# Optimization experiments

Hardware: AMD Instinct MI355X
Metric: run time of the kernel (lower is better)

## Reference

```python
import jax, jax.numpy as jnp
import numpy as np

EPS = 1e-7

def _masked_stats(x, w, k):
    # Parallel equivalent of the sequential Welford update_counter loop:
    # after the loop, mean = running mean, s = sum of squared deviations (M2),
    # std = sqrt(s / (k - 1)). Computed under no_grad in torch -> stop_gradient.
    m = jnp.sum(x * w, axis=0) / k
    s = jnp.sum(w * (x - m) ** 2, axis=0)
    std = jnp.sqrt(s / (k - 1.0))
    return jax.lax.stop_gradient(m), jax.lax.stop_gradient(std)

def _mlp(x, W1, b1, W2, b2):
    # MlpClass(d, d, 2*d, n_hidden=1) with relu act: d -> 2d -> d
    return jax.nn.relu(x @ W1 + b1) @ W2 + b2

def setup_inputs() -> dict:
    key = jax.random.key(0)
    ks = jax.random.split(key, 8)
    B, S, XD, DD = 8, 2048, 1024, 4096
    scale = 0.02
    return {
        "u": jax.random.normal(ks[0], (B, S, XD), jnp.float32),
        "v": jax.random.normal(ks[1], (B, S, DD), jnp.float32),
        "u_W1": jax.random.normal(ks[2], (XD, 2 * XD), jnp.float32) * scale,
        "u_b1": jnp.zeros((2 * XD,), jnp.float32),
        "u_W2": jax.random.normal(ks[3], (2 * XD, XD), jnp.float32) * scale,
        "u_b2": jnp.zeros((XD,), jnp.float32),
        "v_W1": jax.random.normal(ks[4], (DD, 2 * DD), jnp.float32) * scale,
        "v_b1": jnp.zeros((2 * DD,), jnp.float32),
        "v_W2": jax.random.normal(ks[5], (2 * DD, DD), jnp.float32) * scale,
        "v_b2": jnp.zeros((DD,), jnp.float32),
    }

def reference(u, v, u_W1, u_b1, u_W2, u_b2, v_W1, v_b1, v_W2, v_b2):
    u_ = u.reshape(-1, u.shape[-1]).astype(jnp.float32)  # [N, x_dim]
    v_ = v.reshape(-1, v.shape[-1]).astype(jnp.float32)  # [N, delta_dim]
    # nonzero-row mask; torch drops masked rows, we zero them (equivalent math,
    # static shapes). With randn inputs no row is masked.
    nz = jnp.any(u_ != 0, axis=-1) & jnp.any(v_ != 0, axis=-1)
    w = nz.astype(u_.dtype)[:, None]  # [N, 1]
    k = jnp.sum(w)
    u_mean, u_std = _masked_stats(u_, w, k)
    v_mean, v_std = _masked_stats(v_, w, k)
    u_input = (u_ - u_mean) / (u_std + EPS)
    v_input = (v_ - v_mean) / (v_std + EPS)
    out1 = _mlp(u_input, u_W1, u_b1, u_W2, u_b2) * w
    out2 = _mlp(v_input, v_W1, v_b1, v_W2, v_b2) * w
    return out1, out2
```

## Files before the change

### kernel.cpp

```cpp
#include <hip/hip_runtime.h>
#include <hip/hip_bf16.h>

#define NROWS 16384
#define XD 1024
#define DD 4096

typedef __attribute__((ext_vector_type(8))) short short8;
typedef __attribute__((ext_vector_type(4))) float f32x4;

__device__ __forceinline__ unsigned short f2bf(float f) {
  unsigned int u = __builtin_bit_cast(unsigned int, f);
  u += 0x7fffu + ((u >> 16) & 1u);
  return (unsigned short)(u >> 16);
}

__device__ __forceinline__ void load_lds16(const void* g, void* l) {
  __builtin_amdgcn_global_load_lds((const __attribute__((address_space(1))) void*)g,
                                   (__attribute__((address_space(3))) void*)l, 16, 0, 0);
}

__global__ __launch_bounds__(256) void mask_kernel(const float* __restrict__ u,
                                                   const float* __restrict__ v,
                                                   float* __restrict__ w) {
  int r = blockIdx.x;
  int t = threadIdx.x;
  const f32x4* up = (const f32x4*)(u + (size_t)r * XD);
  const f32x4* vp = (const f32x4*)(v + (size_t)r * DD);
  f32x4 a = up[t];
  int fu = __syncthreads_or((a.x != 0.f) | (a.y != 0.f) | (a.z != 0.f) | (a.w != 0.f));
  int fv = 0;
#pragma unroll
  for (int it = 0; it < DD / (256 * 4); ++it) {
    if (!fv) {
      f32x4 b = vp[it * 256 + t];
      fv = __syncthreads_or((b.x != 0.f) | (b.y != 0.f) | (b.z != 0.f) | (b.w != 0.f));
    }
  }
  if (t == 0) w[r] = (fu && fv) ? 1.f : 0.f;
}

__global__ __launch_bounds__(256) void ksum_kernel(const float* __restrict__ w,
                                                   float* __restrict__ kout) {
  __shared__ float sm[256];
  float s = 0.f;
  for (int i = threadIdx.x; i < NROWS; i += 256) s += w[i];
  sm[threadIdx.x] = s;
  __syncthreads();
  for (int st = 128; st > 0; st >>= 1) {
    if (threadIdx.x < st) sm[threadIdx.x] += sm[threadIdx.x + st];
    __syncthreads();
  }
  if (threadIdx.x == 0) kout[0] = sm[0];
}

__global__ __launch_bounds__(256) void colstats_partial(const float* __restrict__ X, int cols,
                                                        const float* __restrict__ w,
                                                        float* __restrict__ p1,
                                                        float* __restrict__ p2) {
  int c = blockIdx.x * 256 + threadIdx.x;
  int r0 = blockIdx.y * (NROWS / 64);
  float s1 = 0.f, s2 = 0.f;
  for (int r = r0; r < r0 + NROWS / 64; ++r) {
    float wr = w[r];
    float x = X[(size_t)r * cols + c];
    float xw = x * wr;
    s1 += xw;
    s2 += xw * x;
  }
  p1[(size_t)blockIdx.y * cols + c] = s1;
  p2[(size_t)blockIdx.y * cols + c] = s2;
}

__global__ __launch_bounds__(256) void colstats_final(const float* __restrict__ p1,
                                                      const float* __restrict__ p2,
                                                      const float* __restrict__ kptr, int cols,
                                                      float* __restrict__ mean,
                                                      float* __restrict__ inv) {
  int c = blockIdx.x * 256 + threadIdx.x;
  float s1 = 0.f, s2 = 0.f;
  for (int j = 0; j < 64; ++j) {
    s1 += p1[(size_t)j * cols + c];
    s2 += p2[(size_t)j * cols + c];
  }
  float k = kptr[0];
  float m = s1 / k;
  float s = s2 - s1 * s1 / k;
  float sd = sqrtf(fmaxf(s, 0.f) / (k - 1.f));
  mean[c] = m;
  inv[c] = 1.f / (sd + 1e-7f);
}

__global__ __launch_bounds__(256) void wt_kernel(const float* __restrict__ W, int R, int C,
                                                 unsigned short* __restrict__ T) {
  __shared__ unsigned short tile[64][65];
  int r0 = blockIdx.x * 64, c0 = blockIdx.y * 64;
  int tr = threadIdx.x >> 2;
  int tc = (threadIdx.x & 3) * 16;
  const float* src = W + (size_t)(r0 + tr) * C + c0 + tc;
#pragma unroll
  for (int i = 0; i < 16; i += 4) {
    f32x4 v4 = *(const f32x4*)(src + i);
    tile[tr][tc + i + 0] = f2bf(v4.x);
    tile[tr][tc + i + 1] = f2bf(v4.y);
    tile[tr][tc + i + 2] = f2bf(v4.z);
    tile[tr][tc + i + 3] = f2bf(v4.w);
  }
  __syncthreads();
  unsigned short* dst = T + (size_t)(c0 + tr) * R + r0 + tc;
  short8 o0, o1;
#pragma unroll
  for (int i = 0; i < 8; ++i) o0[i] = (short)tile[tc + i][tr];
#pragma unroll
  for (int i = 0; i < 8; ++i) o1[i] = (short)tile[tc + 8 + i][tr];
  *(short8*)(dst) = o0;
  *(short8*)(dst + 8) = o1;
}

__global__ __launch_bounds__(256) void norm_kernel(const float* __restrict__ X,
                                                   const float* __restrict__ mean,
                                                   const float* __restrict__ inv,
                                                   unsigned short* __restrict__ O,
                                                   int colmask, size_t n8) {
  size_t stride = (size_t)gridDim.x * 256;
  for (size_t i = (size_t)blockIdx.x * 256 + threadIdx.x; i < n8; i += stride) {
    int c8 = (int)(i & (size_t)colmask);
    const float* xp = X + i * 8;
    f32x4 a = *(const f32x4*)xp;
    f32x4 b = *(const f32x4*)(xp + 4);
    f32x4 m0 = *(const f32x4*)(mean + c8 * 8);
    f32x4 m1 = *(const f32x4*)(mean + c8 * 8 + 4);
    f32x4 i0 = *(const f32x4*)(inv + c8 * 8);
    f32x4 i1 = *(const f32x4*)(inv + c8 * 8 + 4);
    short8 p;
    p[0] = (short)f2bf((a.x - m0.x) * i0.x);
    p[1] = (short)f2bf((a.y - m0.y) * i0.y);
    p[2] = (short)f2bf((a.z - m0.z) * i0.z);
    p[3] = (short)f2bf((a.w - m0.w) * i0.w);
    p[4] = (short)f2bf((b.x - m1.x) * i1.x);
    p[5] = (short)f2bf((b.y - m1.y) * i1.y);
    p[6] = (short)f2bf((b.z - m1.z) * i1.z);
    p[7] = (short)f2bf((b.w - m1.w) * i1.w);
    *(short8*)(O + i * 8) = p;
  }
}

template <int EPI>
__global__ __launch_bounds__(1024, 4) void gemm8p(const unsigned short* __restrict__ A,
                                                  const unsigned short* __restrict__ Bt,
                                                  const float* __restrict__ bias,
                                                  const float* __restrict__ wrow,
                                                  void* __restrict__ OutP,
                                                  int N, int K) {
  __shared__ char lds[131072];
  const int tid = threadIdx.x;
  const int lane = tid & 63;
  const int wave = tid >> 6;
  const int wm = wave >> 2;
  const int wn = wave & 3;

  const int gn = N >> 8;
  const int nwg = gridDim.x;
  const int gm = nwg / gn;
  const int bid = blockIdx.x;
  const int sw = (nwg & 7) ? bid : ((bid & 7) * (nwg >> 3) + (bid >> 3));
  const int SW_W = (gn >= 8) ? 8 : gn;
  const int SW_H = 32 / SW_W;
  int mt, nt;
  if ((gn % SW_W) == 0 && (gm % SW_H) == 0) {
    const int stn = gn / SW_W;
    const int st = sw >> 5;
    const int wi = sw & 31;
    mt = (st / stn) * SW_H + wi / SW_W;
    nt = (st % stn) * SW_W + wi % SW_W;
  } else {
    mt = sw / gn;
    nt = sw % gn;
  }
  const int m0 = mt << 8;
  const int n0 = nt << 8;

  const int srow = tid >> 3;
  const int scol = (((tid & 7) ^ (srow & 7)) << 3);

  const int NT = K >> 6;
  f32x4 acc[4][4] = {};

  const int fr = lane & 15;
  const int kbyte = (lane >> 4) << 4;

#define STAGE(T, BUF)                                                                   \
  {                                                                                     \
    const int k0_ = (T) << 6;                                                           \
    _Pragma("unroll") for (int i = 0; i < 2; ++i) {                                     \
      const int row_ = srow + i * 128;                                                  \
      load_lds16(A + (size_t)(m0 + row_) * K + k0_ + scol,                              \
                 lds + (BUF)*65536 + i * 16384 + tid * 16);                             \
      load_lds16(Bt + (size_t)(n0 + row_) * K + k0_ + scol,                             \
                 lds + (BUF)*65536 + 32768 + i * 16384 + tid * 16);                     \
    }                                                                                   \
  }

  STAGE(0, 0);
  __syncthreads();

  short8 af[4], bf_[4];
  for (int t = 0; t < NT; ++t) {
    const int buf = t & 1;
    const char* Ab = lds + buf * 65536;
    const char* Bb = lds + buf * 65536 + 32768;
    if (t + 1 < NT) STAGE(t + 1, buf ^ 1);

#pragma unroll
    for (int s = 0; s < 2; ++s) {
#pragma unroll
      for (int f = 0; f < 4; ++f) {
        const int r = wm * 64 + f * 16 + fr;
        af[f] = *(const short8*)(Ab + r * 128 + ((s * 64 + kbyte) ^ ((r & 7) << 4)));
      }
#pragma unroll
      for (int g = 0; g < 4; ++g) {
        const int r = wn * 64 + g * 16 + fr;
        bf_[g] = *(const short8*)(Bb + r * 128 + ((s * 64 + kbyte) ^ ((r & 7) << 4)));
      }
      __builtin_amdgcn_s_setprio(1);
#pragma unroll
      for (int f = 0; f < 4; ++f)
#pragma unroll
        for (int g = 0; g < 4; ++g)
          acc[f][g] = __builtin_amdgcn_mfma_f32_16x16x32_bf16(af[f], bf_[g], acc[f][g], 0, 0, 0);
      __builtin_amdgcn_s_setprio(0);
    }
    __syncthreads();
  }
#undef STAGE

  const int colloc = wn * 64 + fr;
  const int rowb = wm * 64 + ((lane >> 4) << 2);
  if (EPI == 0) {
    unsigned short* H = (unsigned short*)OutP;
#pragma unroll
    for (int f = 0; f < 4; ++f)
#pragma unroll
      for (int g = 0; g < 4; ++g) {
        const int c = n0 + colloc + g * 16;
        const float b = bias[c];
#pragma unroll
        for (int r = 0; r < 4; ++r) {
          const int row = m0 + rowb + f * 16 + r;
          H[(size_t)row * N + c] = f2bf(fmaxf(acc[f][g][r] + b, 0.f));
        }
      }
  } else {
    float* O = (float*)OutP;
#pragma unroll
    for (int f = 0; f < 4; ++f)
#pragma unroll
      for (int g = 0; g < 4; ++g) {
        const int c = n0 + colloc + g * 16;
        const float b = bias[c];
#pragma unroll
        for (int r = 0; r < 4; ++r) {
          const int row = m0 + rowb + f * 16 + r;
          O[(size_t)row * N + c] = (acc[f][g][r] + b) * wrow[row];
        }
      }
  }
}

extern "C" void kernel_launch(void* const* d_in, const int* in_sizes, int n_in,
                              void* d_out, int out_size, void* d_ws, size_t ws_size,
                              hipStream_t stream) {
  const float* u    = (const float*)d_in[0];
  const float* v    = (const float*)d_in[1];
  const float* u_W1 = (const float*)d_in[2];
  const float* u_b1 = (const float*)d_in[3];
  const float* u_W2 = (const float*)d_in[4];
  const float* u_b2 = (const float*)d_in[5];
  const float* v_W1 = (const float*)d_in[6];
  const float* v_b1 = (const float*)d_in[7];
  const float* v_W2 = (const float*)d_in[8];
  const float* v_b2 = (const float*)d_in[9];
  float* out1 = (float*)d_out;
  float* out2 = out1 + (size_t)NROWS * XD;

  float* wsf = (float*)d_ws;
  size_t off = 0;
  float* w_     = wsf + off; off += NROWS;
  float* kv     = wsf + off; off += 16;
  float* u_mean = wsf + off; off += XD;
  float* u_inv  = wsf + off; off += XD;
  float* v_mean = wsf + off; off += DD;
  float* v_inv  = wsf + off; off += DD;
  float* p1u    = wsf + off; off += 64 * XD;
  float* p2u    = wsf + off; off += 64 * XD;
  float* p1v    = wsf + off; off += 64 * DD;
  float* p2v    = wsf + off; off += 64 * DD;

  size_t boff = (off * 4 + 255) & ~(size_t)255;
  unsigned short* W1Tu = (unsigned short*)((char*)d_ws + boff); boff += (size_t)(2 * XD) * XD * 2;
  unsigned short* W2Tu = (unsigned short*)((char*)d_ws + boff); boff += (size_t)XD * (2 * XD) * 2;
  unsigned short* W1Tv = (unsigned short*)((char*)d_ws + boff); boff += (size_t)(2 * DD) * DD * 2;
  unsigned short* W2Tv = (unsigned short*)((char*)d_ws + boff); boff += (size_t)DD * (2 * DD) * 2;
  size_t fixedB = (boff + 255) & ~(size_t)255;

  static const int chs[7] = {16384, 8192, 4096, 2048, 1024, 512, 256};
  int CHu = 256, CHv = 256;
  double best = 1e30;
  for (int a = 0; a < 7; ++a)
    for (int b = 0; b < 7; ++b) {
      int cu = chs[a], cv = chs[b];
      size_t need = fixedB + (size_t)cu * XD * 6 + (size_t)cv * DD * 6 + 1024;
      if (need > ws_size) continue;
      auto util = [](int nwg) { return nwg >= 256 ? 1.0 : nwg / 256.0; };
      double cost = 68.75 / util((cu >> 8) * 8) + 68.75 / util((cu >> 8) * 4) +
                    550.0 / util((cv >> 8) * 32) + 550.0 / util((cv >> 8) * 16);
      if (cost < best) { best = cost; CHu = cu; CHv = cv; }
    }

  size_t p = fixedB;
  unsigned short* unc  = (unsigned short*)((char*)d_ws + p); p += (size_t)CHu * XD * 2;
  unsigned short* uhid = (unsigned short*)((char*)d_ws + p); p += (size_t)CHu * (2 * XD) * 2;
  unsigned short* vnc  = (unsigned short*)((char*)d_ws + p); p += (size_t)CHv * DD * 2;
  unsigned short* vhid = (unsigned short*)((char*)d_ws + p);

  mask_kernel<<<NROWS, 256, 0, stream>>>(u, v, w_);
  ksum_kernel<<<1, 256, 0, stream>>>(w_, kv);
  colstats_partial<<<dim3(XD / 256, 64), 256, 0, stream>>>(u, XD, w_, p1u, p2u);
  colstats_partial<<<dim3(DD / 256, 64), 256, 0, stream>>>(v, DD, w_, p1v, p2v);
  colstats_final<<<XD / 256, 256, 0, stream>>>(p1u, p2u, kv, XD, u_mean, u_inv);
  colstats_final<<<DD / 256, 256, 0, stream>>>(p1v, p2v, kv, DD, v_mean, v_inv);

  wt_kernel<<<dim3(XD / 64, (2 * XD) / 64), 256, 0, stream>>>(u_W1, XD, 2 * XD, W1Tu);
  wt_kernel<<<dim3((2 * XD) / 64, XD / 64), 256, 0, stream>>>(u_W2, 2 * XD, XD, W2Tu);
  wt_kernel<<<dim3(DD / 64, (2 * DD) / 64), 256, 0, stream>>>(v_W1, DD, 2 * DD, W1Tv);
  wt_kernel<<<dim3((2 * DD) / 64, DD / 64), 256, 0, stream>>>(v_W2, 2 * DD, DD, W2Tv);

  for (int r0 = 0; r0 < NROWS; r0 += CHu) {
    size_t n8 = (size_t)CHu * XD / 8;
    int ng = (int)(n8 / 256 < 2048 ? n8 / 256 : 2048);
    norm_kernel<<<ng, 256, 0, stream>>>(u + (size_t)r0 * XD, u_mean, u_inv, unc, XD / 8 - 1, n8);
    gemm8p<0><<<(CHu >> 8) * ((2 * XD) >> 8), 1024, 0, stream>>>(unc, W1Tu, u_b1, nullptr, uhid,
                                                                 2 * XD, XD);
    gemm8p<1><<<(CHu >> 8) * (XD >> 8), 1024, 0, stream>>>(uhid, W2Tu, u_b2, w_ + r0,
                                                           out1 + (size_t)r0 * XD, XD, 2 * XD);
  }
  for (int r0 = 0; r0 < NROWS; r0 += CHv) {
    size_t n8 = (size_t)CHv * DD / 8;
    int ng = (int)(n8 / 256 < 2048 ? n8 / 256 : 2048);
    norm_kernel<<<ng, 256, 0, stream>>>(v + (size_t)r0 * DD, v_mean, v_inv, vnc, DD / 8 - 1, n8);
    gemm8p<0><<<(CHv >> 8) * ((2 * DD) >> 8), 1024, 0, stream>>>(vnc, W1Tv, v_b1, nullptr, vhid,
                                                                 2 * DD, DD);
    gemm8p<1><<<(CHv >> 8) * (DD >> 8), 1024, 0, stream>>>(vhid, W2Tv, v_b2, w_ + r0,
                                                           out2 + (size_t)r0 * DD, DD, 2 * DD);
  }
}
```

Measured before the change: 2.271 ms.

## Load B fragments directly from global memory and remap workgroup tile swizzle

The GEMM kernel stops staging the B (weight) tile through LDS. Each wave now reads its B fragments straight from global memory into registers, which halves LDS use to 64KB per block. The tile-to-workgroup mapping also changes: when possible it uses tall 32-row M strips per N column, so a B tile stays hot in cache across consecutive workgroups. This trades LDS traffic and capacity for global and L2 load latency that the double-buffered loop does not hide for B.

```diff
diff --git a/kernel.cpp b/kernel.cpp
--- a/kernel.cpp
+++ b/kernel.cpp
@@ -145,13 +145,13 @@
 }
 
 template <int EPI>
-__global__ __launch_bounds__(1024, 4) void gemm8p(const unsigned short* __restrict__ A,
+__global__ __launch_bounds__(1024, 4) void gemmbg(const unsigned short* __restrict__ A,
                                                   const unsigned short* __restrict__ Bt,
                                                   const float* __restrict__ bias,
                                                   const float* __restrict__ wrow,
                                                   void* __restrict__ OutP,
                                                   int N, int K) {
-  __shared__ char lds[131072];
+  __shared__ char lds[65536];
   const int tid = threadIdx.x;
   const int lane = tid & 63;
   const int wave = tid >> 6;
@@ -163,15 +163,18 @@
   const int gm = nwg / gn;
   const int bid = blockIdx.x;
   const int sw = (nwg & 7) ? bid : ((bid & 7) * (nwg >> 3) + (bid >> 3));
-  const int SW_W = (gn >= 8) ? 8 : gn;
-  const int SW_H = 32 / SW_W;
   int mt, nt;
-  if ((gn % SW_W) == 0 && (gm % SW_H) == 0) {
-    const int stn = gn / SW_W;
+  if ((nwg & 7) == 0 && (gm & 31) == 0) {
     const int st = sw >> 5;
     const int wi = sw & 31;
-    mt = (st / stn) * SW_H + wi / SW_W;
-    nt = (st % stn) * SW_W + wi % SW_W;
+    mt = (st / gn) * 32 + wi;
+    nt = st % gn;
+  } else if ((nwg & 7) == 0 && (gn & 7) == 0 && (gm & 3) == 0) {
+    const int stn = gn >> 3;
+    const int st = sw >> 5;
+    const int wi = sw & 31;
+    mt = (st / stn) * 4 + (wi >> 3);
+    nt = (st % stn) * 8 + (wi & 7);
   } else {
     mt = sw / gn;
     nt = sw % gn;
@@ -187,6 +190,7 @@
 
   const int fr = lane & 15;
   const int kbyte = (lane >> 4) << 4;
+  const unsigned short* bbase = Bt + (size_t)(n0 + wn * 64 + fr) * K + ((lane >> 4) << 3);
 
 #define STAGE(T, BUF)                                                                   \
   {                                                                                     \
@@ -194,9 +198,7 @@
     _Pragma("unroll") for (int i = 0; i < 2; ++i) {                                     \
       const int row_ = srow + i * 128;                                                  \
       load_lds16(A + (size_t)(m0 + row_) * K + k0_ + scol,                              \
-                 lds + (BUF)*65536 + i * 16384 + tid * 16);                             \
-      load_lds16(Bt + (size_t)(n0 + row_) * K + k0_ + scol,                             \
-                 lds + (BUF)*65536 + 32768 + i * 16384 + tid * 16);                     \
+                 lds + (BUF)*32768 + i * 16384 + tid * 16);                             \
     }                                                                                   \
   }
 
@@ -206,21 +208,18 @@
   short8 af[4], bf_[4];
   for (int t = 0; t < NT; ++t) {
     const int buf = t & 1;
-    const char* Ab = lds + buf * 65536;
-    const char* Bb = lds + buf * 65536 + 32768;
+    const char* Ab = lds + buf * 32768;
     if (t + 1 < NT) STAGE(t + 1, buf ^ 1);
 
 #pragma unroll
     for (int s = 0; s < 2; ++s) {
+#pragma unroll
+      for (int g = 0; g < 4; ++g)
+        bf_[g] = *(const short8*)(bbase + (size_t)(g * 16) * K + ((t << 6) + s * 32));
 #pragma unroll
       for (int f = 0; f < 4; ++f) {
         const int r = wm * 64 + f * 16 + fr;
         af[f] = *(const short8*)(Ab + r * 128 + ((s * 64 + kbyte) ^ ((r & 7) << 4)));
-      }
-#pragma unroll
-      for (int g = 0; g < 4; ++g) {
-        const int r = wn * 64 + g * 16 + fr;
-        bf_[g] = *(const short8*)(Bb + r * 128 + ((s * 64 + kbyte) ^ ((r & 7) << 4)));
       }
       __builtin_amdgcn_s_setprio(1);
 #pragma unroll
@@ -339,18 +338,18 @@
     size_t n8 = (size_t)CHu * XD / 8;
     int ng = (int)(n8 / 256 < 2048 ? n8 / 256 : 2048);
     norm_kernel<<<ng, 256, 0, stream>>>(u + (size_t)r0 * XD, u_mean, u_inv, unc, XD / 8 - 1, n8);
-    gemm8p<0><<<(CHu >> 8) * ((2 * XD) >> 8), 1024, 0, stream>>>(unc, W1Tu, u_b1, nullptr, uhid,
+    gemmbg<0><<<(CHu >> 8) * ((2 * XD) >> 8), 1024, 0, stream>>>(unc, W1Tu, u_b1, nullptr, uhid,
                                                                  2 * XD, XD);
-    gemm8p<1><<<(CHu >> 8) * (XD >> 8), 1024, 0, stream>>>(uhid, W2Tu, u_b2, w_ + r0,
+    gemmbg<1><<<(CHu >> 8) * (XD >> 8), 1024, 0, stream>>>(uhid, W2Tu, u_b2, w_ + r0,
                                                            out1 + (size_t)r0 * XD, XD, 2 * XD);
   }
   for (int r0 = 0; r0 < NROWS; r0 += CHv) {
     size_t n8 = (size_t)CHv * DD / 8;
     int ng = (int)(n8 / 256 < 2048 ? n8 / 256 : 2048);
     norm_kernel<<<ng, 256, 0, stream>>>(v + (size_t)r0 * DD, v_mean, v_inv, vnc, DD / 8 - 1, n8);
-    gemm8p<0><<<(CHv >> 8) * ((2 * DD) >> 8), 1024, 0, stream>>>(vnc, W1Tv, v_b1, nullptr, vhid,
+    gemmbg<0><<<(CHv >> 8) * ((2 * DD) >> 8), 1024, 0, stream>>>(vnc, W1Tv, v_b1, nullptr, vhid,
                                                                  2 * DD, DD);
-    gemm8p<1><<<(CHv >> 8) * (DD >> 8), 1024, 0, stream>>>(vhid, W2Tv, v_b2, w_ + r0,
+    gemmbg<1><<<(CHv >> 8) * (DD >> 8), 1024, 0, stream>>>(vhid, W2Tv, v_b2, w_ + r0,
                                                            out2 + (size_t)r0 * DD, DD, 2 * DD);
   }
 }
```

Measured after the change: 5.525 ms. 143% more time.

## Replace 256x256 GEMM tile with 256x128 tile, K-step 32, 512 threads

Applied to the files above, without the earlier changes.

The bf16 MFMA GEMM moves from 1024-thread 256x256 tiles with a 64-wide K step and 128KB LDS to 512-thread 256x128 tiles with a 32-wide K step and 48KB LDS. It also adds a new LDS swizzle and row interleave for the smaller K slice. The goal is more workgroups per GPU and more resident blocks per CU for better occupancy and latency hiding. The chunk-size cost model is updated for the doubled grid. The trade-off is lower arithmetic intensity per tile, more global traffic for A, and twice as many K iterations, each followed by a barrier.

```diff
diff --git a/kernel.cpp b/kernel.cpp
--- a/kernel.cpp
+++ b/kernel.cpp
@@ -145,20 +145,20 @@
 }
 
 template <int EPI>
-__global__ __launch_bounds__(1024, 4) void gemm8p(const unsigned short* __restrict__ A,
-                                                  const unsigned short* __restrict__ Bt,
-                                                  const float* __restrict__ bias,
-                                                  const float* __restrict__ wrow,
-                                                  void* __restrict__ OutP,
-                                                  int N, int K) {
-  __shared__ char lds[131072];
+__global__ __launch_bounds__(512, 4) void gemm2b(const unsigned short* __restrict__ A,
+                                                 const unsigned short* __restrict__ Bt,
+                                                 const float* __restrict__ bias,
+                                                 const float* __restrict__ wrow,
+                                                 void* __restrict__ OutP,
+                                                 int N, int K) {
+  __shared__ char lds[49152];
   const int tid = threadIdx.x;
   const int lane = tid & 63;
   const int wave = tid >> 6;
-  const int wm = wave >> 2;
-  const int wn = wave & 3;
-
-  const int gn = N >> 8;
+  const int wm = wave >> 1;
+  const int wn = wave & 1;
+
+  const int gn = N >> 7;
   const int nwg = gridDim.x;
   const int gm = nwg / gn;
   const int bid = blockIdx.x;
@@ -177,27 +177,27 @@
     nt = sw % gn;
   }
   const int m0 = mt << 8;
-  const int n0 = nt << 8;
-
-  const int srow = tid >> 3;
-  const int scol = (((tid & 7) ^ (srow & 7)) << 3);
-
-  const int NT = K >> 6;
+  const int n0 = nt << 7;
+
+  const int srow = 2 * (tid >> 3) + ((tid >> 2) & 1);
+  const int sksl = (((tid & 3) ^ ((tid >> 3) & 3)) << 3);
+
+  const int NT = K >> 5;
   f32x4 acc[4][4] = {};
 
   const int fr = lane & 15;
-  const int kbyte = (lane >> 4) << 4;
-
-#define STAGE(T, BUF)                                                                   \
-  {                                                                                     \
-    const int k0_ = (T) << 6;                                                           \
-    _Pragma("unroll") for (int i = 0; i < 2; ++i) {                                     \
-      const int row_ = srow + i * 128;                                                  \
-      load_lds16(A + (size_t)(m0 + row_) * K + k0_ + scol,                              \
-                 lds + (BUF)*65536 + i * 16384 + tid * 16);                             \
-      load_lds16(Bt + (size_t)(n0 + row_) * K + k0_ + scol,                             \
-                 lds + (BUF)*65536 + 32768 + i * 16384 + tid * 16);                     \
-    }                                                                                   \
+  const int kg = lane >> 4;
+  const int fo = (fr >> 1) * 128 + (fr & 1) * 64 + (((kg ^ ((fr >> 1) & 3))) << 4);
+
+#define STAGE(T, BUF)                                                              \
+  {                                                                                \
+    const int k0_ = (T) << 5;                                                      \
+    load_lds16(A + (size_t)(m0 + srow) * K + k0_ + sksl,                           \
+               lds + (BUF)*16384 + tid * 16);                                      \
+    load_lds16(A + (size_t)(m0 + srow + 128) * K + k0_ + sksl,                     \
+               lds + (BUF)*16384 + 8192 + tid * 16);                               \
+    load_lds16(Bt + (size_t)(n0 + srow) * K + k0_ + sksl,                          \
+               lds + 32768 + (BUF)*8192 + tid * 16);                               \
   }
 
   STAGE(0, 0);
@@ -206,36 +206,27 @@
   short8 af[4], bf_[4];
   for (int t = 0; t < NT; ++t) {
     const int buf = t & 1;
-    const char* Ab = lds + buf * 65536;
-    const char* Bb = lds + buf * 65536 + 32768;
+    const char* Ab = lds + buf * 16384 + wm * 4096;
+    const char* Bb = lds + 32768 + buf * 8192 + wn * 4096;
     if (t + 1 < NT) STAGE(t + 1, buf ^ 1);
 
 #pragma unroll
-    for (int s = 0; s < 2; ++s) {
-#pragma unroll
-      for (int f = 0; f < 4; ++f) {
-        const int r = wm * 64 + f * 16 + fr;
-        af[f] = *(const short8*)(Ab + r * 128 + ((s * 64 + kbyte) ^ ((r & 7) << 4)));
-      }
-#pragma unroll
-      for (int g = 0; g < 4; ++g) {
-        const int r = wn * 64 + g * 16 + fr;
-        bf_[g] = *(const short8*)(Bb + r * 128 + ((s * 64 + kbyte) ^ ((r & 7) << 4)));
-      }
-      __builtin_amdgcn_s_setprio(1);
-#pragma unroll
-      for (int f = 0; f < 4; ++f)
-#pragma unroll
-        for (int g = 0; g < 4; ++g)
-          acc[f][g] = __builtin_amdgcn_mfma_f32_16x16x32_bf16(af[f], bf_[g], acc[f][g], 0, 0, 0);
-      __builtin_amdgcn_s_setprio(0);
-    }
+    for (int f = 0; f < 4; ++f) af[f] = *(const short8*)(Ab + f * 1024 + fo);
+#pragma unroll
+    for (int g = 0; g < 4; ++g) bf_[g] = *(const short8*)(Bb + g * 1024 + fo);
+    __builtin_amdgcn_s_setprio(1);
+#pragma unroll
+    for (int f = 0; f < 4; ++f)
+#pragma unroll
+      for (int g = 0; g < 4; ++g)
+        acc[f][g] = __builtin_amdgcn_mfma_f32_16x16x32_bf16(af[f], bf_[g], acc[f][g], 0, 0, 0);
+    __builtin_amdgcn_s_setprio(0);
     __syncthreads();
   }
 #undef STAGE
 
   const int colloc = wn * 64 + fr;
-  const int rowb = wm * 64 + ((lane >> 4) << 2);
+  const int rowb = wm * 64 + (kg << 2);
   if (EPI == 0) {
     unsigned short* H = (unsigned short*)OutP;
 #pragma unroll
@@ -311,9 +302,9 @@
       int cu = chs[a], cv = chs[b];
       size_t need = fixedB + (size_t)cu * XD * 6 + (size_t)cv * DD * 6 + 1024;
       if (need > ws_size) continue;
-      auto util = [](int nwg) { return nwg >= 256 ? 1.0 : nwg / 256.0; };
-      double cost = 68.75 / util((cu >> 8) * 8) + 68.75 / util((cu >> 8) * 4) +
-                    550.0 / util((cv >> 8) * 32) + 550.0 / util((cv >> 8) * 16);
+      auto util = [](int nwg) { return nwg >= 512 ? 1.0 : nwg / 512.0; };
+      double cost = 68.75 / util((cu >> 8) * 16) + 68.75 / util((cu >> 8) * 8) +
+                    550.0 / util((cv >> 8) * 64) + 550.0 / util((cv >> 8) * 32);
       if (cost < best) { best = cost; CHu = cu; CHv = cv; }
     }
 
@@ -339,18 +330,18 @@
     size_t n8 = (size_t)CHu * XD / 8;
     int ng = (int)(n8 / 256 < 2048 ? n8 / 256 : 2048);
     norm_kernel<<<ng, 256, 0, stream>>>(u + (size_t)r0 * XD, u_mean, u_inv, unc, XD / 8 - 1, n8);
-    gemm8p<0><<<(CHu >> 8) * ((2 * XD) >> 8), 1024, 0, stream>>>(unc, W1Tu, u_b1, nullptr, uhid,
-                                                                 2 * XD, XD);
-    gemm8p<1><<<(CHu >> 8) * (XD >> 8), 1024, 0, stream>>>(uhid, W2Tu, u_b2, w_ + r0,
-                                                           out1 + (size_t)r0 * XD, XD, 2 * XD);
+    gemm2b<0><<<(CHu >> 8) * ((2 * XD) >> 7), 512, 0, stream>>>(unc, W1Tu, u_b1, nullptr, uhid,
+                                                                2 * XD, XD);
+    gemm2b<1><<<(CHu >> 8) * (XD >> 7), 512, 0, stream>>>(uhid, W2Tu, u_b2, w_ + r0,
+                                                          out1 + (size_t)r0 * XD, XD, 2 * XD);
   }
   for (int r0 = 0; r0 < NROWS; r0 += CHv) {
     size_t n8 = (size_t)CHv * DD / 8;
     int ng = (int)(n8 / 256 < 2048 ? n8 / 256 : 2048);
     norm_kernel<<<ng, 256, 0, stream>>>(v + (size_t)r0 * DD, v_mean, v_inv, vnc, DD / 8 - 1, n8);
-    gemm8p<0><<<(CHv >> 8) * ((2 * DD) >> 8), 1024, 0, stream>>>(vnc, W1Tv, v_b1, nullptr, vhid,
-                                                                 2 * DD, DD);
-    gemm8p<1><<<(CHv >> 8) * (DD >> 8), 1024, 0, stream>>>(vhid, W2Tv, v_b2, w_ + r0,
-                                                           out2 + (size_t)r0 * DD, DD, 2 * DD);
-  }
-}
+    gemm2b<0><<<(CHv >> 8) * ((2 * DD) >> 7), 512, 0, stream>>>(vnc, W1Tv, v_b1, nullptr, vhid,
+                                                                2 * DD, DD);
+    gemm2b<1><<<(CHv >> 8) * (DD >> 7), 512, 0, stream>>>(vhid, W2Tv, v_b2, w_ + r0,
+                                                          out2 + (size_t)r0 * DD, DD, 2 * DD);
+  }
+}
```

Measured after the change: 2.601 ms. +14.5%, slower.
